# Kernel optimization log

Hardware: AMD Instinct MI355X
Metric: run time of the kernel (lower is better)

The kernel has to match this reference:

```python
import jax, jax.numpy as jnp
import numpy as np

HD, L, HEADS, C = 128, 4, 4, 32
EG = np.linspace(-3.0, 3.0, 100)


def _ln(x, s, b, eps=1e-5):
    mu = jnp.mean(x, -1, keepdims=True)
    var = jnp.mean((x - mu) ** 2, -1, keepdims=True)
    return (x - mu) / jnp.sqrt(var + eps) * s + b


def _gat(h, e, src, dst, W, asrc, adst, We, aedge, bias):
    # PyG GATConv (shared src/dst lin, edge_dim, add_self_loops with mean fill)
    N = h.shape[0]
    xl = (h @ W).reshape(N, HEADS, C)
    el = (e @ We).reshape(-1, HEADS, C)
    el_full = jnp.concatenate([el, jnp.broadcast_to(el.mean(0), (N, HEADS, C))], 0)
    ar = jnp.arange(N, dtype=src.dtype)
    sf = jnp.concatenate([src, ar])
    df = jnp.concatenate([dst, ar])
    alpha = (xl[sf] * asrc).sum(-1) + (xl[df] * adst).sum(-1) + (el_full * aedge).sum(-1)
    alpha = jnp.where(alpha > 0, alpha, 0.2 * alpha)  # leaky_relu(0.2)
    m = jax.ops.segment_max(alpha, df, num_segments=N)
    ex = jnp.exp(alpha - m[df])
    den = jax.ops.segment_sum(ex, df, num_segments=N)
    w = ex / den[df]
    out = jax.ops.segment_sum(xl[sf] * w[..., None], df, num_segments=N)
    return out.reshape(N, HEADS * C) + bias


def _forward(x, edge_index, edge_attr, batch, GammaL, GammaR, node_w, node_b,
             edgep_w, edgep_b, gat_lin, att_src, att_dst, gat_lin_edge, att_edge,
             gat_bias, ln_s, ln_b, on_w1, on_b1, on_w2, on_b2, cp_w1, cp_b1, cp_w2, cp_b2):
    src, dst = edge_index[0], edge_index[1]
    B, Hs = GammaL.shape
    h = x @ node_w + node_b
    e = edge_attr @ edgep_w + edgep_b
    for i in range(L):
        hc = _gat(h, e, src, dst, gat_lin[i], att_src[i], att_dst[i],
                  gat_lin_edge[i], att_edge[i], gat_bias[i])
        h = _ln(jax.nn.relu(hc) + h, ln_s[i], ln_b[i])
    # --- block Hamiltonian assembly (n_orb = 1) ---
    dna = jnp.any(x != 0, axis=1)          # contact nodes have all-zero features
    mi = dna.astype(jnp.int32)
    cexc = jnp.cumsum(mi) - mi             # exclusive dna rank over all nodes
    per = jax.ops.segment_sum(mi, batch, num_segments=B)
    before = jnp.cumsum(per) - per
    local = cexc - before[batch]           # local dna index within each graph
    onsite = (jax.nn.relu(h @ on_w1 + on_b1) @ on_w2 + on_b2)[:, 0]
    coup = (jax.nn.relu(e @ cp_w1 + cp_b1) @ cp_w2 + cp_b2)[:, 0]
    H = jnp.zeros((B, Hs, Hs), jnp.float32)
    H = H.at[batch, local, local].add(jnp.where(dna, onsite, 0.0))
    em = dna[src] & dna[dst]               # edges fully inside the DNA block
    u, v, be = local[src], local[dst], batch[src]
    cv = jnp.where(em, coup, 0.0)
    H = H.at[be, u, v].add(cv)
    H = H.at[be, v, u].add(cv)             # hermitian (scalar block)
    I = jnp.eye(Hs, dtype=jnp.float32)
    H = H + 1e-6 * I
    # --- NEGF, Frobenius (real-arithmetic) formulation ---
    Eg = jnp.asarray(EG, jnp.float32)
    A = Eg[None, :, None, None] * I - H[:, None]           # [B,E,Hs,Hs]
    gamma = GammaL + GammaR
    Bm = 0.5 * gamma[:, None, :, None] * I + 1e-12 * I     # [B,1,Hs,Hs] diag
    A_inv = jnp.linalg.inv(A)
    Gr_real = jnp.linalg.inv(A + Bm @ A_inv @ Bm)
    Gr_imag = -(A_inv @ Bm) @ Gr_real
    dos = jnp.log10(jnp.maximum(-jnp.einsum('benn->be', Gr_imag) / np.pi, 1e-16))
    G2 = Gr_real ** 2 + Gr_imag ** 2
    T = jnp.einsum('bi,beij,bj->be', GammaL, G2, GammaR)   # Tr(GL G GR Gd)
    T = jnp.log10(jnp.maximum(T, 1e-16))
    return T, dos, H


def setup_inputs() -> dict:
    key = jax.random.key(0)
    ks = jax.random.split(key, 32)
    B, n_dna, n_con = 8, 128, 2
    n_per = n_dna + n_con
    N = B * n_per
    srcs, dsts = [], []
    for g in range(B):
        base = g * n_per
        for i in range(n_con, n_per - 1):
            srcs.append(base + i); dsts.append(base + i + 1)
        for i in range(n_con, n_per - 2):
            srcs.append(base + i); dsts.append(base + i + 2)
        srcs += [base, base + 1]
        dsts += [base + n_con, base + n_per - 1]
    edge_index = jnp.asarray(np.stack([srcs, dsts]), dtype=jnp.int32)
    E = edge_index.shape[1]
    batch = jnp.asarray(np.repeat(np.arange(B), n_per), dtype=jnp.int32)
    contact = np.zeros(N, bool)
    for g in range(B):
        contact[g * n_per] = True
        contact[g * n_per + 1] = True
    x = jax.random.normal(ks[0], (N, 4), jnp.float32) * jnp.asarray(~contact, jnp.float32)[:, None]
    edge_attr = jax.random.normal(ks[1], (E, 5), jnp.float32)
    GammaL = jax.random.uniform(ks[2], (B, n_dna), jnp.float32) * 0.1
    GammaR = jax.random.uniform(ks[3], (B, n_dna), jnp.float32) * 0.1
    p = lambda k, s: jax.random.normal(k, s, jnp.float32) * 0.05
    hd = HD
    return dict(
        x=x, edge_index=edge_index, edge_attr=edge_attr, batch=batch,
        GammaL=GammaL, GammaR=GammaR,
        node_w=p(ks[4], (4, hd)), node_b=jnp.zeros(hd),
        edgep_w=p(ks[5], (5, hd)), edgep_b=jnp.zeros(hd),
        gat_lin=p(ks[6], (L, hd, hd)), att_src=p(ks[7], (L, HEADS, C)),
        att_dst=p(ks[8], (L, HEADS, C)), gat_lin_edge=p(ks[9], (L, hd, hd)),
        att_edge=p(ks[10], (L, HEADS, C)), gat_bias=jnp.zeros((L, hd)),
        ln_s=jnp.ones((L, hd)), ln_b=jnp.zeros((L, hd)),
        on_w1=p(ks[11], (hd, hd // 2)), on_b1=jnp.zeros(hd // 2),
        on_w2=p(ks[12], (hd // 2, 1)), on_b2=jnp.zeros(1),
        cp_w1=p(ks[13], (hd, hd // 2)), cp_b1=jnp.zeros(hd // 2),
        cp_w2=p(ks[14], (hd // 2, 1)), cp_b2=jnp.zeros(1))


def reference(x, edge_index, edge_attr, batch, GammaL, GammaR, node_w, node_b,
              edgep_w, edgep_b, gat_lin, att_src, att_dst, gat_lin_edge, att_edge,
              gat_bias, ln_s, ln_b, on_w1, on_b1, on_w2, on_b2, cp_w1, cp_b1, cp_w2, cp_b2):
    return _forward(x, edge_index, edge_attr, batch, GammaL, GammaR, node_w, node_b,
                    edgep_w, edgep_b, gat_lin, att_src, att_dst, gat_lin_edge, att_edge,
                    gat_bias, ln_s, ln_b, on_w1, on_b1, on_w2, on_b2, cp_w1, cp_b1, cp_w2, cp_b2)
```

## Files before the change

### kernel.cpp

```cpp
#include <hip/hip_runtime.h>

#define HSZ 128
#define NEGRID 100

typedef float v2f __attribute__((ext_vector_type(2)));

__device__ __forceinline__ unsigned encf(float f) {
  unsigned i = __float_as_uint(f);
  return (i & 0x80000000u) ? ~i : (i | 0x80000000u);
}
__device__ __forceinline__ float decf(unsigned u) {
  return (u & 0x80000000u) ? __uint_as_float(u & 0x7fffffffu) : __uint_as_float(~u);
}

__global__ void k_embed(const float* __restrict__ x, const float* __restrict__ ea,
                        const float* __restrict__ nw, const float* __restrict__ nb,
                        const float* __restrict__ ew, const float* __restrict__ eb,
                        float* __restrict__ h, float* __restrict__ e,
                        float* __restrict__ smean, int N, int E) {
  int row = blockIdx.x, c = threadIdx.x;
  if (row == 0 && c < 16) smean[c] = 0.f;
  if (row < N) {
    float acc = nb[c];
#pragma unroll
    for (int k = 0; k < 4; ++k) acc += x[row * 4 + k] * nw[k * 128 + c];
    h[row * 128 + c] = acc;
  } else {
    int ei = row - N;
    float acc = eb[c];
#pragma unroll
    for (int k = 0; k < 5; ++k) acc += ea[ei * 5 + k] * ew[k * 128 + c];
    e[ei * 128 + c] = acc;
  }
}

__global__ void k_gat_lin(const float* __restrict__ h, const float* __restrict__ e,
                          const float* __restrict__ W, const float* __restrict__ We,
                          const float* __restrict__ asrc, const float* __restrict__ adst,
                          const float* __restrict__ aedge,
                          float* __restrict__ xl, float* __restrict__ ssrc,
                          float* __restrict__ sdst, float* __restrict__ sedge,
                          float* __restrict__ smean4, unsigned* __restrict__ menc,
                          float* __restrict__ den, float* __restrict__ outacc,
                          int N, int E) {
  __shared__ float row_lds[128];
  __shared__ float red[128];
  __shared__ float red2[128];
  int row = blockIdx.x, c = threadIdx.x;
  const float* M;
  if (row < N) { row_lds[c] = h[row * 128 + c]; M = W; }
  else         { row_lds[c] = e[(row - N) * 128 + c]; M = We; }
  __syncthreads();
  float acc = 0.f;
  for (int k = 0; k < 128; ++k) acc += row_lds[k] * M[k * 128 + c];
  if (row < N) {
    xl[row * 128 + c] = acc;
    outacc[row * 128 + c] = 0.f;
    if (c < 4) { menc[row * 4 + c] = 0u; den[row * 4 + c] = 0.f; }
    red[c]  = acc * asrc[c];
    red2[c] = acc * adst[c];
    __syncthreads();
    if (c < 8) {
      int hh = c & 3;
      const float* b = (c < 4) ? red : red2;
      float s = 0.f;
      for (int t = 0; t < 32; ++t) s += b[hh * 32 + t];
      if (c < 4) ssrc[row * 4 + hh] = s; else sdst[row * 4 + hh] = s;
    }
  } else {
    int ei = row - N;
    red[c] = acc * aedge[c];
    __syncthreads();
    if (c < 4) {
      float s = 0.f;
      for (int t = 0; t < 32; ++t) s += red[c * 32 + t];
      sedge[ei * 4 + c] = s;
      atomicAdd(&smean4[c], s);
    }
  }
}

__global__ void k_alpha(const float* __restrict__ ssrc, const float* __restrict__ sdst,
                        const float* __restrict__ sedge, const float* __restrict__ smean4,
                        const int* __restrict__ srcI, const int* __restrict__ dstI,
                        float* __restrict__ alpha, unsigned* __restrict__ menc,
                        int N, int E, float invE) {
  int gid = blockIdx.x * 256 + threadIdx.x;
  if (gid >= (E + N) * 4) return;
  int item = gid >> 2, hh = gid & 3;
  float a; int dnode;
  if (item < E) {
    a = ssrc[srcI[item] * 4 + hh] + sdst[dstI[item] * 4 + hh] + sedge[item * 4 + hh];
    dnode = dstI[item];
  } else {
    int n = item - E;
    a = ssrc[n * 4 + hh] + sdst[n * 4 + hh] + smean4[hh] * invE;
    dnode = n;
  }
  a = (a > 0.f) ? a : 0.2f * a;
  alpha[gid] = a;
  atomicMax(&menc[dnode * 4 + hh], encf(a));
}

__global__ void k_scatter(const float* __restrict__ alpha, const unsigned* __restrict__ menc,
                          const float* __restrict__ xl, const int* __restrict__ srcI,
                          const int* __restrict__ dstI, float* __restrict__ den,
                          float* __restrict__ outacc, int N, int E) {
  int item = blockIdx.x, c = threadIdx.x, hh = c >> 5;
  int sn, dn;
  if (item < E) { sn = srcI[item]; dn = dstI[item]; } else { sn = dn = item - E; }
  float m = decf(menc[dn * 4 + hh]);
  float ex = expf(alpha[item * 4 + hh] - m);
  atomicAdd(&outacc[dn * 128 + c], xl[sn * 128 + c] * ex);
  if (c < 4) {
    float ex2 = expf(alpha[item * 4 + c] - decf(menc[dn * 4 + c]));
    atomicAdd(&den[dn * 4 + c], ex2);
  }
}

__global__ void k_norm(const float* __restrict__ outacc, const float* __restrict__ den,
                       const float* __restrict__ bias, const float* __restrict__ lns,
                       const float* __restrict__ lnb, float* __restrict__ h, int N) {
  __shared__ float buf[128];
  int n = blockIdx.x, c = threadIdx.x, hh = c >> 5;
  float v = outacc[n * 128 + c] / den[n * 4 + hh] + bias[c];
  v = fmaxf(v, 0.f) + h[n * 128 + c];
  buf[c] = v;
  __syncthreads();
  for (int s = 64; s > 0; s >>= 1) { if (c < s) buf[c] += buf[c + s]; __syncthreads(); }
  float mean = buf[0] * (1.f / 128.f);
  __syncthreads();
  float dv = v - mean;
  buf[c] = dv * dv;
  __syncthreads();
  for (int s = 64; s > 0; s >>= 1) { if (c < s) buf[c] += buf[c + s]; __syncthreads(); }
  float var = buf[0] * (1.f / 128.f);
  h[n * 128 + c] = dv * (1.0f / sqrtf(var + 1e-5f)) * lns[c] + lnb[c];
}

__global__ void k_mlp(const float* __restrict__ h, const float* __restrict__ e,
                      const float* __restrict__ w1n, const float* __restrict__ b1n,
                      const float* __restrict__ w2n, const float* __restrict__ b2n,
                      const float* __restrict__ w1e, const float* __restrict__ b1e,
                      const float* __restrict__ w2e, const float* __restrict__ b2e,
                      float* __restrict__ onsite, float* __restrict__ coup, int N, int E) {
  int row = blockIdx.x, t = threadIdx.x;
  const float *vec, *w1, *b1, *w2; float b2v;
  if (row < N) { vec = h + (size_t)row * 128; w1 = w1n; b1 = b1n; w2 = w2n; b2v = b2n[0]; }
  else         { vec = e + (size_t)(row - N) * 128; w1 = w1e; b1 = b1e; w2 = w2e; b2v = b2e[0]; }
  float acc = b1[t];
  for (int k = 0; k < 128; ++k) acc += vec[k] * w1[k * 64 + t];
  acc = fmaxf(acc, 0.f) * w2[t];
#pragma unroll
  for (int off = 32; off; off >>= 1) acc += __shfl_down(acc, off);
  if (t == 0) {
    float r = acc + b2v;
    if (row < N) onsite[row] = r; else coup[row - N] = r;
  }
}

__global__ void k_dna(const float* __restrict__ x, const int* __restrict__ batch,
                      int* __restrict__ dna, int* __restrict__ loc, int N, int B) {
  __shared__ int perB[64];
  __shared__ int beforeB[64];
  int l = threadIdx.x;
  perB[l] = 0;
  __syncthreads();
  int chunk = (N + 63) >> 6;
  int s0 = l * chunk, s1 = min(N, s0 + chunk);
  int cnt = 0;
  for (int n = s0; n < s1; ++n) {
    int mi = (x[n * 4 + 0] != 0.f || x[n * 4 + 1] != 0.f ||
              x[n * 4 + 2] != 0.f || x[n * 4 + 3] != 0.f) ? 1 : 0;
    dna[n] = mi;
    cnt += mi;
    if (mi) atomicAdd(&perB[batch[n]], 1);
  }
  __syncthreads();
  int pre = cnt;
#pragma unroll
  for (int off = 1; off < 64; off <<= 1) {
    int o = __shfl_up(pre, off);
    if (l >= off) pre += o;
  }
  int excl = pre - cnt;
  if (l == 0) {
    int run = 0;
    for (int g = 0; g < B; ++g) { beforeB[g] = run; run += perB[g]; }
  }
  __syncthreads();
  int run = excl;
  for (int n = s0; n < s1; ++n) {
    loc[n] = run - beforeB[batch[n]];
    run += dna[n];
  }
}

__global__ void k_hinit(float* __restrict__ H, int total) {
  int idx = blockIdx.x * 256 + threadIdx.x;
  if (idx >= total) return;
  int ij = idx & (HSZ * HSZ - 1);
  H[idx] = ((ij >> 7) == (ij & 127)) ? 1e-6f : 0.f;
}

__global__ void k_hadd(const int* __restrict__ dna, const int* __restrict__ loc,
                       const int* __restrict__ batch, const int* __restrict__ srcI,
                       const int* __restrict__ dstI, const float* __restrict__ onsite,
                       const float* __restrict__ coup, float* __restrict__ H, int N, int E) {
  int item = blockIdx.x * 256 + threadIdx.x;
  if (item >= N + E) return;
  if (item < N) {
    if (dna[item]) atomicAdd(&H[batch[item] * (HSZ * HSZ) + loc[item] * (HSZ + 1)], onsite[item]);
  } else {
    int ei = item - N;
    int s = srcI[ei], d = dstI[ei];
    if (dna[s] && dna[d]) {
      float cv = coup[ei];
      int b = batch[s];
      atomicAdd(&H[b * (HSZ * HSZ) + loc[s] * HSZ + loc[d]], cv);
      atomicAdd(&H[b * (HSZ * HSZ) + loc[d] * HSZ + loc[s]], cv);
    }
  }
}

__global__ __attribute__((amdgpu_flat_work_group_size(1024, 1024), amdgpu_waves_per_eu(8, 8)))
void k_negf(
    const float* __restrict__ Hm, const float* __restrict__ GL, const float* __restrict__ GR,
    float* __restrict__ outT, float* __restrict__ outD) {
  int bid = blockIdx.x;
  int b = bid / NEGRID, eix = bid % NEGRID;
  float Ev = (float)(-3.0 + (6.0 / 99.0) * (double)eix);

  int tid = threadIdx.x;
  int w = tid >> 6, l = tid & 63;
  int c0 = w << 3, r0 = l << 1;

  __shared__ float gl_s[HSZ], gr_s[HSZ], g_s[HSZ];
  __shared__ v2f fcol[2][HSZ];
  __shared__ v2f prow[16 * 8];
  __shared__ float redbuf[32];

  if (tid < HSZ) {
    float a_ = GL[b * HSZ + tid], b_ = GR[b * HSZ + tid];
    gl_s[tid] = a_; gr_s[tid] = b_;
    g_s[tid] = 0.5f * (a_ + b_) + 1e-12f;
  }
  __syncthreads();

  v2f z00, z01, z02, z03, z04, z05, z06, z07;
  v2f z10, z11, z12, z13, z14, z15, z16, z17;
  const float* Hb = Hm + (size_t)b * HSZ * HSZ;
#define INITR(Z0, Z1, Z2, Z3, Z4, Z5, Z6, Z7, RR) do { \
    int r_ = r0 + RR; \
    const float4 hA = *(const float4*)(Hb + r_ * HSZ + c0); \
    const float4 hB = *(const float4*)(Hb + r_ * HSZ + c0 + 4); \
    float gv = g_s[r_]; \
    Z0 = (v2f){((c0 + 0 == r_) ? Ev : 0.f) - hA.x, (c0 + 0 == r_) ? gv : 0.f}; \
    Z1 = (v2f){((c0 + 1 == r_) ? Ev : 0.f) - hA.y, (c0 + 1 == r_) ? gv : 0.f}; \
    Z2 = (v2f){((c0 + 2 == r_) ? Ev : 0.f) - hA.z, (c0 + 2 == r_) ? gv : 0.f}; \
    Z3 = (v2f){((c0 + 3 == r_) ? Ev : 0.f) - hA.w, (c0 + 3 == r_) ? gv : 0.f}; \
    Z4 = (v2f){((c0 + 4 == r_) ? Ev : 0.f) - hB.x, (c0 + 4 == r_) ? gv : 0.f}; \
    Z5 = (v2f){((c0 + 5 == r_) ? Ev : 0.f) - hB.y, (c0 + 5 == r_) ? gv : 0.f}; \
    Z6 = (v2f){((c0 + 6 == r_) ? Ev : 0.f) - hB.z, (c0 + 6 == r_) ? gv : 0.f}; \
    Z7 = (v2f){((c0 + 7 == r_) ? Ev : 0.f) - hB.w, (c0 + 7 == r_) ? gv : 0.f}; \
  } while (0)
  INITR(z00, z01, z02, z03, z04, z05, z06, z07, 0);
  INITR(z10, z11, z12, z13, z14, z15, z16, z17, 1);

  if (w == 0) { fcol[0][r0] = z00; fcol[0][r0 + 1] = z10; }
  if (l == 0) {
    v2f* pw = &prow[w << 3];
    pw[0] = z00; pw[1] = z01; pw[2] = z02; pw[3] = z03;
    pw[4] = z04; pw[5] = z05; pw[6] = z06; pw[7] = z07;
    if (w == 0) pw[0] = (v2f){z00.x + 1.f, z00.y};
  }
  __syncthreads();

  for (int k = 0; k < HSZ; ++k) {
    int par = k & 1, par2 = par ^ 1;
    v2f pv = fcol[par][k];
    float dmag = pv.x * pv.x + pv.y * pv.y;
    float idn = __builtin_amdgcn_rcpf(dmag);
    idn = idn * (2.0f - dmag * idn);
    float dre = pv.x * idn, dim = -pv.y * idn;

    v2f f0 = fcol[par][r0], f1 = fcol[par][r0 + 1];
    float f0x = f0.x - ((r0 == k) ? 1.f : 0.f);
    float f1x = f1.x - ((r0 + 1 == k) ? 1.f : 0.f);
    float fr0 = f0x * dre - f0.y * dim, fi0 = f0x * dim + f0.y * dre;
    float fr1 = f1x * dre - f1.y * dim, fi1 = f1x * dim + f1.y * dre;
    v2f ar0 = (v2f){-fr0, -fr0}, br0 = (v2f){fi0, -fi0};
    v2f ar1 = (v2f){-fr1, -fr1}, br1 = (v2f){fi1, -fi1};

    const v2f* qp = &prow[w << 3];
#define CELP(Z, AR, BR, Q, QS) do { \
      Z = __builtin_elementwise_fma(AR, Q, Z); \
      Z = __builtin_elementwise_fma(BR, QS, Z); \
    } while (0)
    {
      v2f q0 = qp[0], q1 = qp[1], q2 = qp[2], q3 = qp[3];
      v2f s0 = __builtin_shufflevector(q0, q0, 1, 0);
      v2f s1 = __builtin_shufflevector(q1, q1, 1, 0);
      v2f s2 = __builtin_shufflevector(q2, q2, 1, 0);
      v2f s3 = __builtin_shufflevector(q3, q3, 1, 0);
      CELP(z00, ar0, br0, q0, s0); CELP(z01, ar0, br0, q1, s1);
      CELP(z02, ar0, br0, q2, s2); CELP(z03, ar0, br0, q3, s3);
      CELP(z10, ar1, br1, q0, s0); CELP(z11, ar1, br1, q1, s1);
      CELP(z12, ar1, br1, q2, s2); CELP(z13, ar1, br1, q3, s3);
    }
    {
      v2f q4 = qp[4], q5 = qp[5], q6 = qp[6], q7 = qp[7];
      v2f s4 = __builtin_shufflevector(q4, q4, 1, 0);
      v2f s5 = __builtin_shufflevector(q5, q5, 1, 0);
      v2f s6 = __builtin_shufflevector(q6, q6, 1, 0);
      v2f s7 = __builtin_shufflevector(q7, q7, 1, 0);
      CELP(z04, ar0, br0, q4, s4); CELP(z05, ar0, br0, q5, s5);
      CELP(z06, ar0, br0, q6, s6); CELP(z07, ar0, br0, q7, s7);
      CELP(z14, ar1, br1, q4, s4); CELP(z15, ar1, br1, q5, s5);
      CELP(z16, ar1, br1, q6, s6); CELP(z17, ar1, br1, q7, s7);
    }

    int kn = k + 1;
    if (kn < HSZ) {
      bool stgw = (w == (kn >> 3));
      v2f v0 = (v2f){0.f, 0.f}, v1 = v0;
      if (stgw) {
        switch (kn & 7) {
          case 0:  v0 = z00; v1 = z10; break;
          case 1:  v0 = z01; v1 = z11; break;
          case 2:  v0 = z02; v1 = z12; break;
          case 3:  v0 = z03; v1 = z13; break;
          case 4:  v0 = z04; v1 = z14; break;
          case 5:  v0 = z05; v1 = z15; break;
          case 6:  v0 = z06; v1 = z16; break;
          default: v0 = z07; v1 = z17; break;
        }
        fcol[par2][r0] = v0;
        fcol[par2][r0 + 1] = v1;
      }
      bool myl = (l == (kn >> 1));
      v2f* pw = &prow[w << 3];
      if ((kn & 1) == 0) {
        if (myl) {
          pw[0] = z00; pw[1] = z01; pw[2] = z02; pw[3] = z03;
          pw[4] = z04; pw[5] = z05; pw[6] = z06; pw[7] = z07;
        }
      } else {
        if (myl) {
          pw[0] = z10; pw[1] = z11; pw[2] = z12; pw[3] = z13;
          pw[4] = z14; pw[5] = z15; pw[6] = z16; pw[7] = z17;
        }
      }
      if (stgw && myl) {
        v2f t = (kn & 1) ? v1 : v0;
        prow[(w << 3) + (kn & 7)] = (v2f){t.x + 1.f, t.y};
      }
    }
    __syncthreads();
  }

  float gw0 = gr_s[c0 + 0], gw1 = gr_s[c0 + 1], gw2 = gr_s[c0 + 2], gw3 = gr_s[c0 + 3];
  float gw4 = gr_s[c0 + 4], gw5 = gr_s[c0 + 5], gw6 = gr_s[c0 + 6], gw7 = gr_s[c0 + 7];
  float Tacc = 0.f, Dacc = 0.f;
#define ACCR(Z0, Z1, Z2, Z3, Z4, Z5, Z6, Z7, RR) do { \
    int rr_ = r0 + RR; \
    float glv = gl_s[rr_]; \
    float g2; \
    g2 = Z0.x * Z0.x + Z0.y * Z0.y; Tacc += glv * gw0 * g2; if (rr_ == c0 + 0) Dacc += Z0.y; \
    g2 = Z1.x * Z1.x + Z1.y * Z1.y; Tacc += glv * gw1 * g2; if (rr_ == c0 + 1) Dacc += Z1.y; \
    g2 = Z2.x * Z2.x + Z2.y * Z2.y; Tacc += glv * gw2 * g2; if (rr_ == c0 + 2) Dacc += Z2.y; \
    g2 = Z3.x * Z3.x + Z3.y * Z3.y; Tacc += glv * gw3 * g2; if (rr_ == c0 + 3) Dacc += Z3.y; \
    g2 = Z4.x * Z4.x + Z4.y * Z4.y; Tacc += glv * gw4 * g2; if (rr_ == c0 + 4) Dacc += Z4.y; \
    g2 = Z5.x * Z5.x + Z5.y * Z5.y; Tacc += glv * gw5 * g2; if (rr_ == c0 + 5) Dacc += Z5.y; \
    g2 = Z6.x * Z6.x + Z6.y * Z6.y; Tacc += glv * gw6 * g2; if (rr_ == c0 + 6) Dacc += Z6.y; \
    g2 = Z7.x * Z7.x + Z7.y * Z7.y; Tacc += glv * gw7 * g2; if (rr_ == c0 + 7) Dacc += Z7.y; \
  } while (0)
  ACCR(z00, z01, z02, z03, z04, z05, z06, z07, 0);
  ACCR(z10, z11, z12, z13, z14, z15, z16, z17, 1);
#pragma unroll
  for (int off = 32; off; off >>= 1) {
    Tacc += __shfl_xor(Tacc, off);
    Dacc += __shfl_xor(Dacc, off);
  }
  if (l == 0) { redbuf[w] = Tacc; redbuf[16 + w] = Dacc; }
  __syncthreads();
  if (tid == 0) {
    float T = 0.f, D = 0.f;
    for (int v = 0; v < 16; ++v) { T += redbuf[v]; D += redbuf[16 + v]; }
    outT[bid] = log10f(fmaxf(T, 1e-16f));
    outD[bid] = log10f(fmaxf(-D * 0.31830988618379067f, 1e-16f));
  }
}

extern "C" void kernel_launch(void* const* d_in, const int* in_sizes, int n_in,
                              void* d_out, int out_size, void* d_ws, size_t ws_size,
                              hipStream_t stream) {
  const float* x     = (const float*)d_in[0];
  const int*   eidx  = (const int*)d_in[1];
  const float* eattr = (const float*)d_in[2];
  const int*   batch = (const int*)d_in[3];
  const float* GL    = (const float*)d_in[4];
  const float* GR    = (const float*)d_in[5];
  const float* node_w  = (const float*)d_in[6];
  const float* node_b  = (const float*)d_in[7];
  const float* edgep_w = (const float*)d_in[8];
  const float* edgep_b = (const float*)d_in[9];
  const float* gat_lin      = (const float*)d_in[10];
  const float* att_src      = (const float*)d_in[11];
  const float* att_dst      = (const float*)d_in[12];
  const float* gat_lin_edge = (const float*)d_in[13];
  const float* att_edge     = (const float*)d_in[14];
  const float* gat_bias     = (const float*)d_in[15];
  const float* ln_s = (const float*)d_in[16];
  const float* ln_b = (const float*)d_in[17];
  const float* on_w1 = (const float*)d_in[18];
  const float* on_b1 = (const float*)d_in[19];
  const float* on_w2 = (const float*)d_in[20];
  const float* on_b2 = (const float*)d_in[21];
  const float* cp_w1 = (const float*)d_in[22];
  const float* cp_b1 = (const float*)d_in[23];
  const float* cp_w2 = (const float*)d_in[24];
  const float* cp_b2 = (const float*)d_in[25];

  int N = in_sizes[0] / 4;
  int E = in_sizes[1] / 2;
  int B = in_sizes[4] / HSZ;
  const int* srcI = eidx;
  const int* dstI = eidx + E;

  float* ws = (float*)d_ws;
  size_t o = 0;
  float* h     = ws + o; o += (size_t)N * 128;
  float* ebuf  = ws + o; o += (size_t)E * 128;
  float* xl    = ws + o; o += (size_t)N * 128;
  float* ssrc  = ws + o; o += (size_t)N * 4;
  float* sdst  = ws + o; o += (size_t)N * 4;
  float* sedge = ws + o; o += (size_t)E * 4;
  float* smean = ws + o; o += 16;
  float* alpha = ws + o; o += (size_t)(E + N) * 4;
  unsigned* menc = (unsigned*)(ws + o); o += (size_t)N * 4;
  float* den    = ws + o; o += (size_t)N * 4;
  float* outacc = ws + o; o += (size_t)N * 128;
  float* onsite = ws + o; o += (size_t)((N + 3) & ~3);
  float* coup   = ws + o; o += (size_t)((E + 3) & ~3);
  int* dna = (int*)(ws + o); o += (size_t)((N + 3) & ~3);
  int* loc = (int*)(ws + o); o += (size_t)((N + 3) & ~3);

  float* out  = (float*)d_out;
  float* outT = out;
  float* outD = out + (size_t)B * NEGRID;
  float* outH = out + (size_t)2 * B * NEGRID;

  k_embed<<<N + E, 128, 0, stream>>>(x, eattr, node_w, node_b, edgep_w, edgep_b,
                                     h, ebuf, smean, N, E);
  for (int l = 0; l < 4; ++l) {
    k_gat_lin<<<N + E, 128, 0, stream>>>(
        h, ebuf, gat_lin + (size_t)l * 16384, gat_lin_edge + (size_t)l * 16384,
        att_src + l * 128, att_dst + l * 128, att_edge + l * 128,
        xl, ssrc, sdst, sedge, smean + l * 4, menc, den, outacc, N, E);
    int items = (E + N) * 4;
    k_alpha<<<(items + 255) / 256, 256, 0, stream>>>(
        ssrc, sdst, sedge, smean + l * 4, srcI, dstI, alpha, menc, N, E, 1.0f / (float)E);
    k_scatter<<<E + N, 128, 0, stream>>>(alpha, menc, xl, srcI, dstI, den, outacc, N, E);
    k_norm<<<N, 128, 0, stream>>>(outacc, den, gat_bias + l * 128,
                                  ln_s + l * 128, ln_b + l * 128, h, N);
  }
  k_mlp<<<N + E, 64, 0, stream>>>(h, ebuf, on_w1, on_b1, on_w2, on_b2,
                                  cp_w1, cp_b1, cp_w2, cp_b2, onsite, coup, N, E);
  k_dna<<<1, 64, 0, stream>>>(x, batch, dna, loc, N, B);
  int htot = B * HSZ * HSZ;
  k_hinit<<<(htot + 255) / 256, 256, 0, stream>>>(outH, htot);
  k_hadd<<<(N + E + 255) / 256, 256, 0, stream>>>(dna, loc, batch, srcI, dstI,
                                                  onsite, coup, outH, N, E);
  k_negf<<<B * NEGRID, 1024, 0, stream>>>(outH, GL, GR, outT, outD);
}
```

Measured before the change: 650.3 us.

## Block Gauss-Jordan inversion by 2x2 pivot blocks to halve barrier count

The in-place complex Gauss-Jordan inversion in the NEGF kernel now eliminates two pivots per iteration using a 2x2 block pivot (Schur-complement style), so it runs 64 steps instead of 128. This halves the number of __syncthreads barriers and shared-memory pivot row/column exchanges, and uses float4 LDS accesses. Each step does more arithmetic per element (four FMAs per component), and pivoting two rows at once may slightly change numerical behavior.

After: 756.7 us. 1.16x slower.

```diff
diff --git a/kernel.cpp b/kernel.cpp
--- a/kernel.cpp
+++ b/kernel.cpp
@@ -236,8 +236,8 @@
   int c0 = w << 3, r0 = l << 1;
 
   __shared__ float gl_s[HSZ], gr_s[HSZ], g_s[HSZ];
-  __shared__ v2f fcol[2][HSZ];
-  __shared__ v2f prow[16 * 8];
+  __shared__ v2f fcol2[2][2][HSZ];
+  __shared__ v2f prow[16 * 16];
   __shared__ float redbuf[32];
 
   if (tid < HSZ) {
@@ -267,93 +267,117 @@
   INITR(z00, z01, z02, z03, z04, z05, z06, z07, 0);
   INITR(z10, z11, z12, z13, z14, z15, z16, z17, 1);
 
-  if (w == 0) { fcol[0][r0] = z00; fcol[0][r0 + 1] = z10; }
+  if (w == 0) {
+    *(float4*)&fcol2[0][0][r0] = make_float4(z00.x, z00.y, z10.x, z10.y);
+    *(float4*)&fcol2[0][1][r0] = make_float4(z01.x, z01.y, z11.x, z11.y);
+  }
   if (l == 0) {
-    v2f* pw = &prow[w << 3];
-    pw[0] = z00; pw[1] = z01; pw[2] = z02; pw[3] = z03;
-    pw[4] = z04; pw[5] = z05; pw[6] = z06; pw[7] = z07;
-    if (w == 0) pw[0] = (v2f){z00.x + 1.f, z00.y};
-  }
-  __syncthreads();
-
-  for (int k = 0; k < HSZ; ++k) {
-    int par = k & 1, par2 = par ^ 1;
-    v2f pv = fcol[par][k];
-    float dmag = pv.x * pv.x + pv.y * pv.y;
-    float idn = __builtin_amdgcn_rcpf(dmag);
-    idn = idn * (2.0f - dmag * idn);
-    float dre = pv.x * idn, dim = -pv.y * idn;
-
-    v2f f0 = fcol[par][r0], f1 = fcol[par][r0 + 1];
-    float f0x = f0.x - ((r0 == k) ? 1.f : 0.f);
-    float f1x = f1.x - ((r0 + 1 == k) ? 1.f : 0.f);
-    float fr0 = f0x * dre - f0.y * dim, fi0 = f0x * dim + f0.y * dre;
-    float fr1 = f1x * dre - f1.y * dim, fi1 = f1x * dim + f1.y * dre;
-    v2f ar0 = (v2f){-fr0, -fr0}, br0 = (v2f){fi0, -fi0};
-    v2f ar1 = (v2f){-fr1, -fr1}, br1 = (v2f){fi1, -fi1};
-
-    const v2f* qp = &prow[w << 3];
-#define CELP(Z, AR, BR, Q, QS) do { \
-      Z = __builtin_elementwise_fma(AR, Q, Z); \
-      Z = __builtin_elementwise_fma(BR, QS, Z); \
+    float4* qw = (float4*)&prow[w * 16];
+    qw[0] = make_float4(z00.x, z00.y, z01.x, z01.y);
+    qw[1] = make_float4(z02.x, z02.y, z03.x, z03.y);
+    qw[2] = make_float4(z04.x, z04.y, z05.x, z05.y);
+    qw[3] = make_float4(z06.x, z06.y, z07.x, z07.y);
+    qw[4] = make_float4(z10.x, z10.y, z11.x, z11.y);
+    qw[5] = make_float4(z12.x, z12.y, z13.x, z13.y);
+    qw[6] = make_float4(z14.x, z14.y, z15.x, z15.y);
+    qw[7] = make_float4(z16.x, z16.y, z17.x, z17.y);
+    if (w == 0) {
+      prow[0] = (v2f){z00.x + 1.f, z00.y};
+      prow[8 + 1] = (v2f){z11.x + 1.f, z11.y};
+    }
+  }
+  __syncthreads();
+
+  for (int t = 0; t < 64; ++t) {
+    int P = t & 1, Pn = P ^ 1;
+    int k0 = 2 * t;
+    float4 ua = *(const float4*)&fcol2[P][0][k0];
+    float4 ub = *(const float4*)&fcol2[P][1][k0];
+    float m0 = ua.x * ua.x + ua.y * ua.y;
+    float i0 = __builtin_amdgcn_rcpf(m0); i0 = i0 * (2.0f - m0 * i0);
+    float dre0 = ua.x * i0, dim0 = -ua.y * i0;
+    float er = dre0 * ub.x - dim0 * ub.y, ei = dre0 * ub.y + dim0 * ub.x;
+    float pr = ub.z - (ua.z * er - ua.w * ei);
+    float pq = ub.w - (ua.z * ei + ua.w * er);
+    float m1 = pr * pr + pq * pq;
+    float i1 = __builtin_amdgcn_rcpf(m1); i1 = i1 * (2.0f - m1 * i1);
+    float dre1 = pr * i1, dim1 = -pq * i1;
+    float hr = dre0 * ua.z - dim0 * ua.w, hi = dre0 * ua.w + dim0 * ua.z;
+
+    float4 ff0 = *(const float4*)&fcol2[P][0][r0];
+    float4 ff1 = *(const float4*)&fcol2[P][1][r0];
+    if (l == t) { ff0.x -= 1.f; ff1.z -= 1.f; }
+    float t1x = ff1.x - (ff0.x * er - ff0.y * ei);
+    float t1y = ff1.y - (ff0.x * ei + ff0.y * er);
+    float G1x0 = t1x * dre1 - t1y * dim1, G1y0 = t1x * dim1 + t1y * dre1;
+    float G0x0 = (ff0.x * dre0 - ff0.y * dim0) - (G1x0 * hr - G1y0 * hi);
+    float G0y0 = (ff0.x * dim0 + ff0.y * dre0) - (G1x0 * hi + G1y0 * hr);
+    float t2x = ff1.z - (ff0.z * er - ff0.w * ei);
+    float t2y = ff1.w - (ff0.z * ei + ff0.w * er);
+    float G1x1 = t2x * dre1 - t2y * dim1, G1y1 = t2x * dim1 + t2y * dre1;
+    float G0x1 = (ff0.z * dre0 - ff0.w * dim0) - (G1x1 * hr - G1y1 * hi);
+    float G0y1 = (ff0.z * dim0 + ff0.w * dre0) - (G1x1 * hi + G1y1 * hr);
+
+    const float4* qa = (const float4*)&prow[w * 16];
+    const float4* qb = (const float4*)&prow[w * 16 + 8];
+#define UPD(Z, G0x, G0y, G1x, G1y, q0x, q0y, q1x, q1y) do { \
+      Z.x = __builtin_fmaf(-(G0x), q0x, __builtin_fmaf( (G0y), q0y, \
+            __builtin_fmaf(-(G1x), q1x, __builtin_fmaf( (G1y), q1y, Z.x)))); \
+      Z.y = __builtin_fmaf(-(G0x), q0y, __builtin_fmaf(-(G0y), q0x, \
+            __builtin_fmaf(-(G1x), q1y, __builtin_fmaf(-(G1y), q1x, Z.y)))); \
     } while (0)
     {
-      v2f q0 = qp[0], q1 = qp[1], q2 = qp[2], q3 = qp[3];
-      v2f s0 = __builtin_shufflevector(q0, q0, 1, 0);
-      v2f s1 = __builtin_shufflevector(q1, q1, 1, 0);
-      v2f s2 = __builtin_shufflevector(q2, q2, 1, 0);
-      v2f s3 = __builtin_shufflevector(q3, q3, 1, 0);
-      CELP(z00, ar0, br0, q0, s0); CELP(z01, ar0, br0, q1, s1);
-      CELP(z02, ar0, br0, q2, s2); CELP(z03, ar0, br0, q3, s3);
-      CELP(z10, ar1, br1, q0, s0); CELP(z11, ar1, br1, q1, s1);
-      CELP(z12, ar1, br1, q2, s2); CELP(z13, ar1, br1, q3, s3);
+      float4 A0 = qa[0], A1 = qa[1], B0 = qb[0], B1 = qb[1];
+      UPD(z00, G0x0, G0y0, G1x0, G1y0, A0.x, A0.y, B0.x, B0.y);
+      UPD(z01, G0x0, G0y0, G1x0, G1y0, A0.z, A0.w, B0.z, B0.w);
+      UPD(z02, G0x0, G0y0, G1x0, G1y0, A1.x, A1.y, B1.x, B1.y);
+      UPD(z03, G0x0, G0y0, G1x0, G1y0, A1.z, A1.w, B1.z, B1.w);
+      UPD(z10, G0x1, G0y1, G1x1, G1y1, A0.x, A0.y, B0.x, B0.y);
+      UPD(z11, G0x1, G0y1, G1x1, G1y1, A0.z, A0.w, B0.z, B0.w);
+      UPD(z12, G0x1, G0y1, G1x1, G1y1, A1.x, A1.y, B1.x, B1.y);
+      UPD(z13, G0x1, G0y1, G1x1, G1y1, A1.z, A1.w, B1.z, B1.w);
     }
     {
-      v2f q4 = qp[4], q5 = qp[5], q6 = qp[6], q7 = qp[7];
-      v2f s4 = __builtin_shufflevector(q4, q4, 1, 0);
-      v2f s5 = __builtin_shufflevector(q5, q5, 1, 0);
-      v2f s6 = __builtin_shufflevector(q6, q6, 1, 0);
-      v2f s7 = __builtin_shufflevector(q7, q7, 1, 0);
-      CELP(z04, ar0, br0, q4, s4); CELP(z05, ar0, br0, q5, s5);
-      CELP(z06, ar0, br0, q6, s6); CELP(z07, ar0, br0, q7, s7);
-      CELP(z14, ar1, br1, q4, s4); CELP(z15, ar1, br1, q5, s5);
-      CELP(z16, ar1, br1, q6, s6); CELP(z17, ar1, br1, q7, s7);
-    }
-
-    int kn = k + 1;
-    if (kn < HSZ) {
-      bool stgw = (w == (kn >> 3));
-      v2f v0 = (v2f){0.f, 0.f}, v1 = v0;
+      float4 A2 = qa[2], A3 = qa[3], B2 = qb[2], B3 = qb[3];
+      UPD(z04, G0x0, G0y0, G1x0, G1y0, A2.x, A2.y, B2.x, B2.y);
+      UPD(z05, G0x0, G0y0, G1x0, G1y0, A2.z, A2.w, B2.z, B2.w);
+      UPD(z06, G0x0, G0y0, G1x0, G1y0, A3.x, A3.y, B3.x, B3.y);
+      UPD(z07, G0x0, G0y0, G1x0, G1y0, A3.z, A3.w, B3.z, B3.w);
+      UPD(z14, G0x1, G0y1, G1x1, G1y1, A2.x, A2.y, B2.x, B2.y);
+      UPD(z15, G0x1, G0y1, G1x1, G1y1, A2.z, A2.w, B2.z, B2.w);
+      UPD(z16, G0x1, G0y1, G1x1, G1y1, A3.x, A3.y, B3.x, B3.y);
+      UPD(z17, G0x1, G0y1, G1x1, G1y1, A3.z, A3.w, B3.z, B3.w);
+    }
+
+    if (t < 63) {
+      int tn = t + 1, wn = tn >> 2, pi = tn & 3;
+      bool stgw = (w == wn);
+      v2f v00 = (v2f){0.f, 0.f}, v11 = v00;
       if (stgw) {
-        switch (kn & 7) {
-          case 0:  v0 = z00; v1 = z10; break;
-          case 1:  v0 = z01; v1 = z11; break;
-          case 2:  v0 = z02; v1 = z12; break;
-          case 3:  v0 = z03; v1 = z13; break;
-          case 4:  v0 = z04; v1 = z14; break;
-          case 5:  v0 = z05; v1 = z15; break;
-          case 6:  v0 = z06; v1 = z16; break;
-          default: v0 = z07; v1 = z17; break;
+        v2f v01, v10;
+        switch (pi) {
+          case 0:  v00 = z00; v01 = z01; v10 = z10; v11 = z11; break;
+          case 1:  v00 = z02; v01 = z03; v10 = z12; v11 = z13; break;
+          case 2:  v00 = z04; v01 = z05; v10 = z14; v11 = z15; break;
+          default: v00 = z06; v01 = z07; v10 = z16; v11 = z17; break;
         }
-        fcol[par2][r0] = v0;
-        fcol[par2][r0 + 1] = v1;
+        *(float4*)&fcol2[Pn][0][r0] = make_float4(v00.x, v00.y, v10.x, v10.y);
+        *(float4*)&fcol2[Pn][1][r0] = make_float4(v01.x, v01.y, v11.x, v11.y);
       }
-      bool myl = (l == (kn >> 1));
-      v2f* pw = &prow[w << 3];
-      if ((kn & 1) == 0) {
-        if (myl) {
-          pw[0] = z00; pw[1] = z01; pw[2] = z02; pw[3] = z03;
-          pw[4] = z04; pw[5] = z05; pw[6] = z06; pw[7] = z07;
+      if (l == tn) {
+        float4* qw = (float4*)&prow[w * 16];
+        qw[0] = make_float4(z00.x, z00.y, z01.x, z01.y);
+        qw[1] = make_float4(z02.x, z02.y, z03.x, z03.y);
+        qw[2] = make_float4(z04.x, z04.y, z05.x, z05.y);
+        qw[3] = make_float4(z06.x, z06.y, z07.x, z07.y);
+        qw[4] = make_float4(z10.x, z10.y, z11.x, z11.y);
+        qw[5] = make_float4(z12.x, z12.y, z13.x, z13.y);
+        qw[6] = make_float4(z14.x, z14.y, z15.x, z15.y);
+        qw[7] = make_float4(z16.x, z16.y, z17.x, z17.y);
+        if (stgw) {
+          prow[w * 16 + 2 * pi] = (v2f){v00.x + 1.f, v00.y};
+          prow[w * 16 + 8 + 2 * pi + 1] = (v2f){v11.x + 1.f, v11.y};
         }
-      } else {
-        if (myl) {
-          pw[0] = z10; pw[1] = z11; pw[2] = z12; pw[3] = z13;
-          pw[4] = z14; pw[5] = z15; pw[6] = z16; pw[7] = z17;
-        }
-      }
-      if (stgw && myl) {
-        v2f t = (kn & 1) ? v1 : v0;
-        prow[(w << 3) + (kn & 7)] = (v2f){t.x + 1.f, t.y};
       }
     }
     __syncthreads();
```
